# Optimization experiments

Measured on AMD Instinct MI355X. Metric: run time of the kernel, lower is better.

## Reference

```python
import jax, jax.numpy as jnp
import numpy as np

B, N, C = 4, 1024, 23          # batch, nodes, scalar input channels (Rs_in=[(23,0)])
NB, H = 3, 100                 # cosine basis size, radial MLP hidden width
MAX_R = 3.0                    # CosineBasisModel max_radius
D1, D2, D3 = 30, 10, 1         # fc1/fc2/fc3 head dims


def setup_inputs() -> dict:
    key = jax.random.key(0)
    ks = jax.random.split(key, 12)
    features = jax.random.normal(ks[0], (B, N, C), jnp.float32)
    # random points inside a box comparable to max_radius so edges hit the basis support
    geometry = jax.random.uniform(ks[1], (B, N, 3), jnp.float32) * MAX_R
    # radial MLP (CosineBasisModel): NB -> H (relu) -> C weights (l=0 -> l=0 path, mul 23*1)
    W_rb1 = jax.random.normal(ks[2], (NB, H), jnp.float32) / np.sqrt(NB)
    b_rb1 = jnp.zeros((H,), jnp.float32)
    W_rb2 = jax.random.normal(ks[3], (H, C), jnp.float32) / np.sqrt(H)
    b_rb2 = jnp.zeros((C,), jnp.float32)
    # dense MLP head: Linear(N,30) -> Linear(30,10) -> Linear(10,1)
    W_fc1 = jax.random.normal(ks[4], (N, D1), jnp.float32) / np.sqrt(N)
    b_fc1 = jnp.zeros((D1,), jnp.float32)
    W_fc2 = jax.random.normal(ks[5], (D1, D2), jnp.float32) / np.sqrt(D1)
    b_fc2 = jnp.zeros((D2,), jnp.float32)
    W_fc3 = jax.random.normal(ks[6], (D2, D3), jnp.float32) / np.sqrt(D2)
    b_fc3 = jnp.zeros((D3,), jnp.float32)
    return {
        "features": features, "geometry": geometry,
        "W_rb1": W_rb1, "b_rb1": b_rb1, "W_rb2": W_rb2, "b_rb2": b_rb2,
        "W_fc1": W_fc1, "b_fc1": b_fc1, "W_fc2": W_fc2, "b_fc2": b_fc2,
        "W_fc3": W_fc3, "b_fc3": b_fc3,
    }


def _cosine_basis(r):
    """e3nn CosineBasisModel basis: cos^2 bumps centered on linspace(0,max_r,NB). r: [...]->[...,NB]."""
    radii = jnp.linspace(0.0, MAX_R, NB, dtype=r.dtype)
    step = radii[1] - radii[0]
    u = (r[..., None] - radii) / step
    half_pi = jnp.asarray(np.pi / 2, r.dtype)
    return jnp.where(jnp.abs(u) < 1.0, jnp.cos(half_pi * u) ** 2, jnp.zeros_like(u))


def reference(features, geometry, W_rb1, b_rb1, W_rb2, b_rb2,
              W_fc1, b_fc1, W_fc2, b_fc2, W_fc3, b_fc3):
    diff = geometry[:, :, None, :] - geometry[:, None, :, :]      # [B,N,N,3]
    r = jnp.sqrt(jnp.sum(diff * diff, axis=-1) + 1e-12)           # [B,N,N]
    basis = _cosine_basis(r)                                      # [B,N,N,NB]
    h = jax.nn.relu(basis @ W_rb1 + b_rb1)                        # [B,N,N,H]
    w = h @ W_rb2 + b_rb2                                         # [B,N,N,C] per-edge radial weights
    # scatter-sum weighted neighbor features -> scalar per node, 1/sqrt(N) kernel norm
    conv = jnp.einsum('zabc,zbc->za', w, features) / jnp.sqrt(jnp.asarray(N, w.dtype))  # [B,N]
    x = jax.nn.relu(conv @ W_fc1 + b_fc1)                         # [B,30]
    x = jax.nn.relu(x @ W_fc2 + b_fc2)                            # [B,10]
    x = x @ W_fc3 + b_fc3                                         # [B,1]
    return x
```

## Files before the change

### kernel.cpp

```cpp
#include <hip/hip_runtime.h>

#define Nn 1024
#define Cc 23
#define Hh 100
#define KN 64
#define DSTR 68
#define MUSCALE 14.0f
#define MUCLAMP 62.999f
#define NBC 2048

#define UT_OFF     0
#define G4_OFF     1536
#define WF1T_OFF   17920
#define BIAS_OFF   48640
#define COLSUM_OFF 48644
#define D_OFF      48704
#define PB_OFF     310912
#define X1PRE_OFF  372352

__device__ __forceinline__ float rdlane(float v, int l) {
    return __int_as_float(__builtin_amdgcn_readlane(__float_as_int(v), l));
}

__global__ __launch_bounds__(256)
void prep_kernel(const float* __restrict__ f,
                 const float* __restrict__ geom,
                 const float* __restrict__ W1,
                 const float* __restrict__ b1,
                 const float* __restrict__ W2,
                 const float* __restrict__ b2,
                 const float* __restrict__ Wf1,
                 float* __restrict__ ws) {
    int blk = blockIdx.x;
    int t = threadIdx.x;
    if (blk < 64) {
        __shared__ float w2s[Hh * Cc];
        __shared__ float hv_s[Hh];
        int k = blk;
        for (int j = t; j < Hh * Cc; j += 256) w2s[j] = W2[j];
        if (t < Hh) {
            float v = (float)k * (3.0f / 63.0f);
            const float HPI = 1.57079632679f;
            float c0 = cosf(HPI * v);
            float c1 = cosf(HPI * (v - 1.0f));
            float c2 = cosf(HPI * (v - 2.0f));
            float s0 = (v < 1.0f) ? c0 * c0 : 0.0f;
            float s1 = (fabsf(v - 1.0f) < 1.0f) ? c1 * c1 : 0.0f;
            float s2 = (v > 1.0f && v < 3.0f) ? c2 * c2 : 0.0f;
            float pre = fmaf(s0, W1[t],
                         fmaf(s1, W1[Hh + t],
                          fmaf(s2, W1[2 * Hh + t], b1[t])));
            hv_s[t] = fmaxf(pre, 0.f);
        }
        __syncthreads();
        if (t < Cc) {
            float a0 = 0.f, a1 = 0.f;
            #pragma unroll 4
            for (int h = 0; h < Hh; h += 2) {
                a0 = fmaf(hv_s[h],     w2s[h * Cc + t],       a0);
                a1 = fmaf(hv_s[h + 1], w2s[(h + 1) * Cc + t], a1);
            }
            ws[UT_OFF + t * KN + k] = a0 + a1;
        }
    } else if (blk < 80) {
        int zb = (blk - 64) * 256 + t;
        const float* g = geom + zb * 3;
        reinterpret_cast<float4*>(ws + G4_OFF)[zb] =
            make_float4(g[0], g[1], g[2], 0.f);
    } else if (blk < 84) {
        __shared__ float red[256];
        int z = blk - 80;
        float s = 0.f;
        #pragma unroll
        for (int rr = 0; rr < 4; ++rr) {
            const float* fr = f + ((z << 10) + rr * 256 + t) * Cc;
            #pragma unroll
            for (int c = 0; c < Cc; ++c) s = fmaf(fr[c], b2[c], s);
        }
        red[t] = s; __syncthreads();
        for (int off = 128; off; off >>= 1) {
            if (t < off) red[t] += red[t + off];
            __syncthreads();
        }
        if (t == 0) ws[BIAS_OFF + z] = red[0];
    } else if (blk == 84) {
        __shared__ float cs_s[240];
        if (t < 240) {
            int d = t % 30, oct = t / 30;
            float c0 = 0.f, c1 = 0.f;
            #pragma unroll 4
            for (int j = 0; j < 128; j += 2) {
                c0 += Wf1[(oct * 128 + j) * 30 + d];
                c1 += Wf1[(oct * 128 + j + 1) * 30 + d];
            }
            cs_s[t] = c0 + c1;
        }
        __syncthreads();
        if (t < 30) {
            float cs = 0.f;
            #pragma unroll
            for (int o = 0; o < 8; ++o) cs += cs_s[o * 30 + t];
            ws[COLSUM_OFF + t] = cs;
        }
    } else {
        int d = blk - 85;
        #pragma unroll
        for (int j = 0; j < 4; ++j) {
            int k = j * 256 + t;
            ws[WF1T_OFF + d * Nn + k] = Wf1[k * 30 + d] * 0.03125f;
        }
    }
}

__global__ __launch_bounds__(256)
void dgemm_kernel(const float* __restrict__ f,
                  const float* __restrict__ ut,
                  float* __restrict__ D) {
    const int t = threadIdx.x;
    const int lane = t & 63;
    const int wv = __builtin_amdgcn_readfirstlane(t >> 6);
    float ur[Cc];
    #pragma unroll
    for (int c = 0; c < Cc; ++c) ur[c] = ut[c * KN + lane];
    const int row0 = blockIdx.x * 16 + wv * 4;
    float fr[2];
    {
        int base = row0 * Cc;
        fr[0] = f[base + lane];
        int o2 = 64 + lane; if (o2 > 91) o2 = 91;
        fr[1] = f[base + o2];
    }
    #pragma unroll
    for (int r = 0; r < 4; ++r) {
        float a0 = 0.f, a1 = 0.f, a2 = 0.f, a3 = 0.f;
        #pragma unroll
        for (int c = 0; c < 20; c += 4) {
            a0 = fmaf(rdlane(fr[(r * Cc + c + 0) >> 6], (r * Cc + c + 0) & 63), ur[c + 0], a0);
            a1 = fmaf(rdlane(fr[(r * Cc + c + 1) >> 6], (r * Cc + c + 1) & 63), ur[c + 1], a1);
            a2 = fmaf(rdlane(fr[(r * Cc + c + 2) >> 6], (r * Cc + c + 2) & 63), ur[c + 2], a2);
            a3 = fmaf(rdlane(fr[(r * Cc + c + 3) >> 6], (r * Cc + c + 3) & 63), ur[c + 3], a3);
        }
        a0 = fmaf(rdlane(fr[(r * Cc + 20) >> 6], (r * Cc + 20) & 63), ur[20], a0);
        a1 = fmaf(rdlane(fr[(r * Cc + 21) >> 6], (r * Cc + 21) & 63), ur[21], a1);
        a2 = fmaf(rdlane(fr[(r * Cc + 22) >> 6], (r * Cc + 22) & 63), ur[22], a2);
        D[(row0 + r) * KN + lane] = (a0 + a1) + (a2 + a3);
    }
}

__global__ __launch_bounds__(128, 4)
void conv_kernel(const float* __restrict__ geom,
                 const float* __restrict__ Dg,
                 const float4* __restrict__ geom4,
                 const float2* __restrict__ wf1t2,
                 float* __restrict__ pb) {
    __shared__ float lds_d[16 * DSTR];
    __shared__ float lds_acc[128];
    const int bid = blockIdx.x;
    const int t = threadIdx.x;
    const int lane = t & 63;
    const int wv = __builtin_amdgcn_readfirstlane(t >> 6);
    const int z = bid >> 9;
    const int ah = (bid >> 6) & 7;
    const int s = bid & 63;
    const int b0 = s * 16;

    {
        const float4* src = reinterpret_cast<const float4*>(Dg + ((z << 10) + b0) * KN);
        #pragma unroll
        for (int j = t; j < 256; j += 128) {
            int row = j >> 4, k4 = j & 15;
            reinterpret_cast<float4*>(lds_d)[row * 17 + k4] = src[j];
        }
    }
    float gr;
    {
        int off = lane < 48 ? lane : 47;
        gr = geom[((z << 10) + b0) * 3 + off];
    }
    float4 ga = geom4[(z << 10) + (ah << 7) + t];
    __syncthreads();

    float acc = 0.f;
    #pragma unroll
    for (int bl = 0; bl < 16; ++bl) {
        float dx = ga.x - rdlane(gr, bl * 3 + 0);
        float dy = ga.y - rdlane(gr, bl * 3 + 1);
        float dz = ga.z - rdlane(gr, bl * 3 + 2);
        float r = sqrtf(fmaf(dx, dx, fmaf(dy, dy, fmaf(dz, dz, 1e-12f))));
        float mu = fminf(r * MUSCALE, MUCLAMP);
        int m = (int)mu;
        float tt = mu - (float)m;
        const float* row = lds_d + bl * DSTR + m;
        float d0 = row[0];
        float d1 = row[1];
        acc += fmaf(tt, d1 - d0, d0);
    }
    lds_acc[t] = acc;
    __syncthreads();

    {
        const float2* a2 = reinterpret_cast<const float2*>(lds_acc);
        float2 av = a2[lane];
        #pragma unroll
        for (int i = 0; i < 15; ++i) {
            int d = wv * 15 + i;
            float2 w = wf1t2[d * 512 + (ah << 6) + lane];
            float sum = av.x * w.x + av.y * w.y;
            #pragma unroll
            for (int off = 32; off; off >>= 1) sum += __shfl_down(sum, off);
            if (lane == 0) pb[d * NBC + (z << 9) + (ah << 6) + s] = sum;
        }
    }
}

__global__ __launch_bounds__(256)
void head1_kernel(const float* __restrict__ pb,
                  float* __restrict__ x1pre) {
    int d = blockIdx.x;
    int t = threadIdx.x;
    int z = t >> 6, lane = t & 63;
    const float4* p4 = reinterpret_cast<const float4*>(pb + d * NBC + (z << 9));
    float4 v0 = p4[lane * 2];
    float4 v1 = p4[lane * 2 + 1];
    float s = ((v0.x + v0.y) + (v0.z + v0.w)) + ((v1.x + v1.y) + (v1.z + v1.w));
    #pragma unroll
    for (int off = 32; off; off >>= 1) s += __shfl_down(s, off);
    if (lane == 0) x1pre[d * 4 + z] = s;
}

__global__ __launch_bounds__(128)
void fc23_kernel(const float* __restrict__ ws,
                 const float* __restrict__ bf1,
                 const float* __restrict__ Wf2, const float* __restrict__ bf2,
                 const float* __restrict__ Wf3, const float* __restrict__ bf3,
                 float* __restrict__ out) {
    __shared__ float x1s[120];
    __shared__ float x2s[40];
    int t = threadIdx.x;
    if (t < 120) {
        int d = t >> 2, zz = t & 3;
        float x1 = ws[X1PRE_OFF + t]
                 + ws[BIAS_OFF + zz] * 0.03125f * ws[COLSUM_OFF + d]
                 + bf1[d];
        x1s[zz * 30 + d] = fmaxf(x1, 0.f);
    }
    __syncthreads();
    if (t < 40) {
        int zz = t / 10, d = t % 10;
        float sm = bf2[d];
        #pragma unroll
        for (int kk = 0; kk < 30; ++kk)
            sm = fmaf(x1s[zz * 30 + kk], Wf2[kk * 10 + d], sm);
        x2s[t] = fmaxf(sm, 0.f);
    }
    __syncthreads();
    if (t < 4) {
        float sm = bf3[0];
        #pragma unroll
        for (int kk = 0; kk < 10; ++kk)
            sm = fmaf(x2s[t * 10 + kk], Wf3[kk], sm);
        out[t] = sm;
    }
}

extern "C" void kernel_launch(void* const* d_in, const int* in_sizes, int n_in,
                              void* d_out, int out_size, void* d_ws, size_t ws_size,
                              hipStream_t stream) {
    const float* f   = (const float*)d_in[0];
    const float* geo = (const float*)d_in[1];
    const float* W1  = (const float*)d_in[2];
    const float* b1  = (const float*)d_in[3];
    const float* W2  = (const float*)d_in[4];
    const float* b2  = (const float*)d_in[5];
    const float* Wf1 = (const float*)d_in[6];
    const float* bf1 = (const float*)d_in[7];
    const float* Wf2 = (const float*)d_in[8];
    const float* bf2 = (const float*)d_in[9];
    const float* Wf3 = (const float*)d_in[10];
    const float* bf3 = (const float*)d_in[11];
    float* ws  = (float*)d_ws;
    float* out = (float*)d_out;

    hipLaunchKernelGGL(prep_kernel, dim3(115), dim3(256), 0, stream,
                       f, geo, W1, b1, W2, b2, Wf1, ws);
    hipLaunchKernelGGL(dgemm_kernel, dim3(256), dim3(256), 0, stream,
                       f, ws + UT_OFF, ws + D_OFF);
    hipLaunchKernelGGL(conv_kernel, dim3(NBC), dim3(128), 0, stream,
                       geo, ws + D_OFF,
                       reinterpret_cast<const float4*>(ws + G4_OFF),
                       reinterpret_cast<const float2*>(ws + WF1T_OFF),
                       ws + PB_OFF);
    hipLaunchKernelGGL(head1_kernel, dim3(30), dim3(256), 0, stream,
                       ws + PB_OFF, ws + X1PRE_OFF);
    hipLaunchKernelGGL(fc23_kernel, dim3(1), dim3(128), 0, stream,
                       ws, bf1, Wf2, bf2, Wf3, bf3, out);
}
```

Measured before the change: 27.43 us.

## Regroup pipeline stages to cut kernel launches from five to four

Splits the radial-table computation into its own small kernel and fuses the feature GEMM with the bias, column-sum and weight-transpose prep into one auxiliary kernel. The two head kernels (per-d reduction and fc2/fc3) are merged into one 512-thread single-block kernel. The padded float4 geometry copy is dropped, so the conv kernel reads raw xyz with three scalar loads. The aim is to remove launch and dependency gaps, at the cost of a serial reduction in one block for the head and less coalesced geometry loads.

```diff
diff --git a/kernel.cpp b/kernel.cpp
--- a/kernel.cpp
+++ b/kernel.cpp
@@ -10,66 +10,94 @@
 #define NBC 2048
 
 #define UT_OFF     0
-#define G4_OFF     1536
-#define WF1T_OFF   17920
-#define BIAS_OFF   48640
-#define COLSUM_OFF 48644
-#define D_OFF      48704
-#define PB_OFF     310912
-#define X1PRE_OFF  372352
+#define WF1T_OFF   1536
+#define BIAS_OFF   32256
+#define COLSUM_OFF 32260
+#define D_OFF      32320
+#define PB_OFF     294464
 
 __device__ __forceinline__ float rdlane(float v, int l) {
     return __int_as_float(__builtin_amdgcn_readlane(__float_as_int(v), l));
 }
 
 __global__ __launch_bounds__(256)
-void prep_kernel(const float* __restrict__ f,
-                 const float* __restrict__ geom,
-                 const float* __restrict__ W1,
-                 const float* __restrict__ b1,
-                 const float* __restrict__ W2,
-                 const float* __restrict__ b2,
-                 const float* __restrict__ Wf1,
-                 float* __restrict__ ws) {
+void ut_kernel(const float* __restrict__ W1,
+               const float* __restrict__ b1,
+               const float* __restrict__ W2,
+               float* __restrict__ ws) {
+    __shared__ float w2s[Hh * Cc];
+    __shared__ float hv_s[Hh];
+    int k = blockIdx.x;
+    int t = threadIdx.x;
+    for (int j = t; j < Hh * Cc; j += 256) w2s[j] = W2[j];
+    if (t < Hh) {
+        float v = (float)k * (3.0f / 63.0f);
+        const float HPI = 1.57079632679f;
+        float c0 = cosf(HPI * v);
+        float c1 = cosf(HPI * (v - 1.0f));
+        float c2 = cosf(HPI * (v - 2.0f));
+        float s0 = (v < 1.0f) ? c0 * c0 : 0.0f;
+        float s1 = (fabsf(v - 1.0f) < 1.0f) ? c1 * c1 : 0.0f;
+        float s2 = (v > 1.0f && v < 3.0f) ? c2 * c2 : 0.0f;
+        float pre = fmaf(s0, W1[t],
+                     fmaf(s1, W1[Hh + t],
+                      fmaf(s2, W1[2 * Hh + t], b1[t])));
+        hv_s[t] = fmaxf(pre, 0.f);
+    }
+    __syncthreads();
+    if (t < Cc) {
+        float a0 = 0.f, a1 = 0.f;
+        #pragma unroll 4
+        for (int h = 0; h < Hh; h += 2) {
+            a0 = fmaf(hv_s[h],     w2s[h * Cc + t],       a0);
+            a1 = fmaf(hv_s[h + 1], w2s[(h + 1) * Cc + t], a1);
+        }
+        ws[UT_OFF + t * KN + k] = a0 + a1;
+    }
+}
+
+__global__ __launch_bounds__(256)
+void aux_kernel(const float* __restrict__ f,
+                const float* __restrict__ W1,
+                const float* __restrict__ b2,
+                const float* __restrict__ Wf1,
+                float* __restrict__ ws) {
     int blk = blockIdx.x;
     int t = threadIdx.x;
-    if (blk < 64) {
-        __shared__ float w2s[Hh * Cc];
-        __shared__ float hv_s[Hh];
-        int k = blk;
-        for (int j = t; j < Hh * Cc; j += 256) w2s[j] = W2[j];
-        if (t < Hh) {
-            float v = (float)k * (3.0f / 63.0f);
-            const float HPI = 1.57079632679f;
-            float c0 = cosf(HPI * v);
-            float c1 = cosf(HPI * (v - 1.0f));
-            float c2 = cosf(HPI * (v - 2.0f));
-            float s0 = (v < 1.0f) ? c0 * c0 : 0.0f;
-            float s1 = (fabsf(v - 1.0f) < 1.0f) ? c1 * c1 : 0.0f;
-            float s2 = (v > 1.0f && v < 3.0f) ? c2 * c2 : 0.0f;
-            float pre = fmaf(s0, W1[t],
-                         fmaf(s1, W1[Hh + t],
-                          fmaf(s2, W1[2 * Hh + t], b1[t])));
-            hv_s[t] = fmaxf(pre, 0.f);
-        }
-        __syncthreads();
-        if (t < Cc) {
-            float a0 = 0.f, a1 = 0.f;
-            #pragma unroll 4
-            for (int h = 0; h < Hh; h += 2) {
-                a0 = fmaf(hv_s[h],     w2s[h * Cc + t],       a0);
-                a1 = fmaf(hv_s[h + 1], w2s[(h + 1) * Cc + t], a1);
+    if (blk < 256) {
+        const int lane = t & 63;
+        const int wv = __builtin_amdgcn_readfirstlane(t >> 6);
+        const float* ut = ws + UT_OFF;
+        float ur[Cc];
+        #pragma unroll
+        for (int c = 0; c < Cc; ++c) ur[c] = ut[c * KN + lane];
+        const int row0 = blk * 16 + wv * 4;
+        float fr[2];
+        {
+            int base = row0 * Cc;
+            fr[0] = f[base + lane];
+            int o2 = 64 + lane; if (o2 > 91) o2 = 91;
+            fr[1] = f[base + o2];
+        }
+        float* D = ws + D_OFF;
+        #pragma unroll
+        for (int r = 0; r < 4; ++r) {
+            float a0 = 0.f, a1 = 0.f, a2 = 0.f, a3 = 0.f;
+            #pragma unroll
+            for (int c = 0; c < 20; c += 4) {
+                a0 = fmaf(rdlane(fr[(r * Cc + c + 0) >> 6], (r * Cc + c + 0) & 63), ur[c + 0], a0);
+                a1 = fmaf(rdlane(fr[(r * Cc + c + 1) >> 6], (r * Cc + c + 1) & 63), ur[c + 1], a1);
+                a2 = fmaf(rdlane(fr[(r * Cc + c + 2) >> 6], (r * Cc + c + 2) & 63), ur[c + 2], a2);
+                a3 = fmaf(rdlane(fr[(r * Cc + c + 3) >> 6], (r * Cc + c + 3) & 63), ur[c + 3], a3);
             }
-            ws[UT_OFF + t * KN + k] = a0 + a1;
-        }
-    } else if (blk < 80) {
-        int zb = (blk - 64) * 256 + t;
-        const float* g = geom + zb * 3;
-        reinterpret_cast<float4*>(ws + G4_OFF)[zb] =
-            make_float4(g[0], g[1], g[2], 0.f);
-    } else if (blk < 84) {
+            a0 = fmaf(rdlane(fr[(r * Cc + 20) >> 6], (r * Cc + 20) & 63), ur[20], a0);
+            a1 = fmaf(rdlane(fr[(r * Cc + 21) >> 6], (r * Cc + 21) & 63), ur[21], a1);
+            a2 = fmaf(rdlane(fr[(r * Cc + 22) >> 6], (r * Cc + 22) & 63), ur[22], a2);
+            D[(row0 + r) * KN + lane] = (a0 + a1) + (a2 + a3);
+        }
+    } else if (blk < 260) {
         __shared__ float red[256];
-        int z = blk - 80;
+        int z = blk - 256;
         float s = 0.f;
         #pragma unroll
         for (int rr = 0; rr < 4; ++rr) {
@@ -83,7 +111,7 @@
             __syncthreads();
         }
         if (t == 0) ws[BIAS_OFF + z] = red[0];
-    } else if (blk == 84) {
+    } else if (blk == 260) {
         __shared__ float cs_s[240];
         if (t < 240) {
             int d = t % 30, oct = t / 30;
@@ -103,7 +131,7 @@
             ws[COLSUM_OFF + t] = cs;
         }
     } else {
-        int d = blk - 85;
+        int d = blk - 261;
         #pragma unroll
         for (int j = 0; j < 4; ++j) {
             int k = j * 256 + t;
@@ -112,45 +140,9 @@
     }
 }
 
-__global__ __launch_bounds__(256)
-void dgemm_kernel(const float* __restrict__ f,
-                  const float* __restrict__ ut,
-                  float* __restrict__ D) {
-    const int t = threadIdx.x;
-    const int lane = t & 63;
-    const int wv = __builtin_amdgcn_readfirstlane(t >> 6);
-    float ur[Cc];
-    #pragma unroll
-    for (int c = 0; c < Cc; ++c) ur[c] = ut[c * KN + lane];
-    const int row0 = blockIdx.x * 16 + wv * 4;
-    float fr[2];
-    {
-        int base = row0 * Cc;
-        fr[0] = f[base + lane];
-        int o2 = 64 + lane; if (o2 > 91) o2 = 91;
-        fr[1] = f[base + o2];
-    }
-    #pragma unroll
-    for (int r = 0; r < 4; ++r) {
-        float a0 = 0.f, a1 = 0.f, a2 = 0.f, a3 = 0.f;
-        #pragma unroll
-        for (int c = 0; c < 20; c += 4) {
-            a0 = fmaf(rdlane(fr[(r * Cc + c + 0) >> 6], (r * Cc + c + 0) & 63), ur[c + 0], a0);
-            a1 = fmaf(rdlane(fr[(r * Cc + c + 1) >> 6], (r * Cc + c + 1) & 63), ur[c + 1], a1);
-            a2 = fmaf(rdlane(fr[(r * Cc + c + 2) >> 6], (r * Cc + c + 2) & 63), ur[c + 2], a2);
-            a3 = fmaf(rdlane(fr[(r * Cc + c + 3) >> 6], (r * Cc + c + 3) & 63), ur[c + 3], a3);
-        }
-        a0 = fmaf(rdlane(fr[(r * Cc + 20) >> 6], (r * Cc + 20) & 63), ur[20], a0);
-        a1 = fmaf(rdlane(fr[(r * Cc + 21) >> 6], (r * Cc + 21) & 63), ur[21], a1);
-        a2 = fmaf(rdlane(fr[(r * Cc + 22) >> 6], (r * Cc + 22) & 63), ur[22], a2);
-        D[(row0 + r) * KN + lane] = (a0 + a1) + (a2 + a3);
-    }
-}
-
 __global__ __launch_bounds__(128, 4)
 void conv_kernel(const float* __restrict__ geom,
                  const float* __restrict__ Dg,
-                 const float4* __restrict__ geom4,
                  const float2* __restrict__ wf1t2,
                  float* __restrict__ pb) {
     __shared__ float lds_d[16 * DSTR];
@@ -177,15 +169,16 @@
         int off = lane < 48 ? lane : 47;
         gr = geom[((z << 10) + b0) * 3 + off];
     }
-    float4 ga = geom4[(z << 10) + (ah << 7) + t];
+    const int ag = (z << 10) + (ah << 7) + t;
+    float gax = geom[ag * 3], gay = geom[ag * 3 + 1], gaz = geom[ag * 3 + 2];
     __syncthreads();
 
     float acc = 0.f;
     #pragma unroll
     for (int bl = 0; bl < 16; ++bl) {
-        float dx = ga.x - rdlane(gr, bl * 3 + 0);
-        float dy = ga.y - rdlane(gr, bl * 3 + 1);
-        float dz = ga.z - rdlane(gr, bl * 3 + 2);
+        float dx = gax - rdlane(gr, bl * 3 + 0);
+        float dy = gay - rdlane(gr, bl * 3 + 1);
+        float dz = gaz - rdlane(gr, bl * 3 + 2);
         float r = sqrtf(fmaf(dx, dx, fmaf(dy, dy, fmaf(dz, dz, 1e-12f))));
         float mu = fminf(r * MUSCALE, MUCLAMP);
         int m = (int)mu;
@@ -213,33 +206,34 @@
     }
 }
 
-__global__ __launch_bounds__(256)
-void head1_kernel(const float* __restrict__ pb,
-                  float* __restrict__ x1pre) {
-    int d = blockIdx.x;
-    int t = threadIdx.x;
-    int z = t >> 6, lane = t & 63;
-    const float4* p4 = reinterpret_cast<const float4*>(pb + d * NBC + (z << 9));
-    float4 v0 = p4[lane * 2];
-    float4 v1 = p4[lane * 2 + 1];
-    float s = ((v0.x + v0.y) + (v0.z + v0.w)) + ((v1.x + v1.y) + (v1.z + v1.w));
-    #pragma unroll
-    for (int off = 32; off; off >>= 1) s += __shfl_down(s, off);
-    if (lane == 0) x1pre[d * 4 + z] = s;
-}
-
-__global__ __launch_bounds__(128)
-void fc23_kernel(const float* __restrict__ ws,
+__global__ __launch_bounds__(512)
+void head_kernel(const float* __restrict__ ws,
                  const float* __restrict__ bf1,
                  const float* __restrict__ Wf2, const float* __restrict__ bf2,
                  const float* __restrict__ Wf3, const float* __restrict__ bf3,
                  float* __restrict__ out) {
+    __shared__ float tb[480];
     __shared__ float x1s[120];
     __shared__ float x2s[40];
     int t = threadIdx.x;
+    if (t < 480) {
+        int d = t >> 4, rem = t & 15;
+        int z = rem >> 2, q = rem & 3;
+        const float4* p4 = reinterpret_cast<const float4*>(
+            ws + PB_OFF + d * NBC + (z << 9) + q * 128);
+        float s0 = 0.f, s1 = 0.f, s2 = 0.f, s3 = 0.f;
+        #pragma unroll
+        for (int j = 0; j < 32; ++j) {
+            float4 v = p4[j];
+            s0 += v.x; s1 += v.y; s2 += v.z; s3 += v.w;
+        }
+        tb[t] = (s0 + s1) + (s2 + s3);
+    }
+    __syncthreads();
     if (t < 120) {
         int d = t >> 2, zz = t & 3;
-        float x1 = ws[X1PRE_OFF + t]
+        int base = d * 16 + zz * 4;
+        float x1 = ((tb[base] + tb[base + 1]) + (tb[base + 2] + tb[base + 3]))
                  + ws[BIAS_OFF + zz] * 0.03125f * ws[COLSUM_OFF + d]
                  + bf1[d];
         x1s[zz * 30 + d] = fmaxf(x1, 0.f);
@@ -281,17 +275,14 @@
     float* ws  = (float*)d_ws;
     float* out = (float*)d_out;
 
-    hipLaunchKernelGGL(prep_kernel, dim3(115), dim3(256), 0, stream,
-                       f, geo, W1, b1, W2, b2, Wf1, ws);
-    hipLaunchKernelGGL(dgemm_kernel, dim3(256), dim3(256), 0, stream,
-                       f, ws + UT_OFF, ws + D_OFF);
+    hipLaunchKernelGGL(ut_kernel, dim3(64), dim3(256), 0, stream,
+                       W1, b1, W2, ws);
+    hipLaunchKernelGGL(aux_kernel, dim3(291), dim3(256), 0, stream,
+                       f, W1, b2, Wf1, ws);
     hipLaunchKernelGGL(conv_kernel, dim3(NBC), dim3(128), 0, stream,
                        geo, ws + D_OFF,
-                       reinterpret_cast<const float4*>(ws + G4_OFF),
                        reinterpret_cast<const float2*>(ws + WF1T_OFF),
                        ws + PB_OFF);
-    hipLaunchKernelGGL(head1_kernel, dim3(30), dim3(256), 0, stream,
-                       ws + PB_OFF, ws + X1PRE_OFF);
-    hipLaunchKernelGGL(fc23_kernel, dim3(1), dim3(128), 0, stream,
+    hipLaunchKernelGGL(head_kernel, dim3(1), dim3(512), 0, stream,
                        ws, bf1, Wf2, bf2, Wf3, bf3, out);
 }
```

Measured after the change: 36.95 us. 34.7% more time.
